# Performance work log

Hardware: AMD Instinct MI355X
Metric: run time of the kernel (lower is better)

## Reference

```python
import jax, jax.numpy as jnp
import numpy as np

B, S, D, H, HD, F, V = 16, 512, 256, 8, 32, 682, 32000
EPS = 1.1920928955078125e-07


def rmsnorm(x, w):
    return x * jax.lax.rsqrt(jnp.mean(x * x, axis=-1, keepdims=True) + EPS) * w


def rope(x, cos, sin):
    # interleaved RoPE: even/odd lanes rotated pairwise, re-interleaved
    xe, xo = x[..., ::2], x[..., 1::2]
    return jnp.stack([xe * cos - xo * sin, xe * sin + xo * cos], axis=-1).reshape(x.shape)


def setup_inputs() -> dict:
    key = jax.random.key(0)
    ks = jax.random.split(key, 12)
    def n(k, shape, s=0.02):
        return jax.random.normal(k, shape, jnp.float32) * s
    pos = jnp.arange(S, dtype=jnp.float32)
    inv = 1.0 / (10000.0 ** (jnp.arange(0, HD, 2, dtype=jnp.float32) / HD))
    ang = pos[:, None] * inv[None, :]                      # [S, HD/2]
    cos_tab = jnp.repeat(jnp.cos(ang), 2, axis=-1)         # [S, HD]
    sin_tab = jnp.repeat(jnp.sin(ang), 2, axis=-1)
    mask = jnp.tril(jnp.ones((S, S), jnp.int32))[None, None]  # causal [1,1,S,S]
    return dict(
        emb=n(ks[0], (V, D)),
        pos_emb=n(ks[1], (S, D)),
        attn_norm_w=jnp.ones((D,), jnp.float32),
        wq=n(ks[2], (D, D)), bq=jnp.zeros((D,), jnp.float32),
        wk=n(ks[3], (HD, D)), bk=jnp.zeros((HD,), jnp.float32),
        wv=n(ks[4], (D, D)), bv=jnp.zeros((D,), jnp.float32),
        cos_tab=cos_tab, sin_tab=sin_tab,
        ffn_norm_w=jnp.ones((D,), jnp.float32),
        w_gate=n(ks[5], (F, D)), b_gate=jnp.zeros((F,), jnp.float32),
        w_up=n(ks[6], (F, D)), b_up=jnp.zeros((F,), jnp.float32),
        w_down=n(ks[7], (D, F)), b_down=jnp.zeros((D,), jnp.float32),
        tok_ids=jax.random.randint(ks[8], (B, S), 0, V, jnp.int64),
        mask=mask,
    )


def reference(emb, pos_emb, attn_norm_w, wq, bq, wk, bk, wv, bv, cos_tab, sin_tab,
              ffn_norm_w, w_gate, b_gate, w_up, b_up, w_down, b_down, tok_ids, mask):
    h = emb[tok_ids] + pos_emb                                   # [B,S,D]
    x = rmsnorm(h, attn_norm_w)
    # faithful to trace: direct view [B,S,D] -> [B,H,S,HD] (no transpose)
    q = (x @ wq.T + bq).reshape(B, H, S, HD)
    k = (x @ wk.T + bk)[:, None]                                 # [B,1,S,HD] single KV head
    v = (x @ wv.T + bv).reshape(B, H, S, HD)
    cos = cos_tab[:S, ::2][None, None]                           # [1,1,S,HD/2]
    sin = sin_tab[:S, ::2][None, None]
    qr = rope(q, cos, sin)
    kr = rope(k, cos, sin)[:, 0]                                 # [B,S,HD]
    scores = jnp.einsum('bhsd,btd->bhst', qr, kr) / jnp.sqrt(jnp.float32(HD))
    scores = jnp.where(mask == 0, -jnp.inf, scores)
    attn = jax.nn.softmax(scores, axis=-1)
    o = jnp.einsum('bhst,bhtd->bhsd', attn, v).reshape(B, S, D)
    h2 = o + h
    x2 = rmsnorm(h2, ffn_norm_w)
    g = x2 @ w_gate.T + b_gate
    g = g * jax.nn.sigmoid(g)                                    # SiLU gate
    up = x2 @ w_up.T + b_up
    out = (g * up) @ w_down.T + b_down
    # faithful to trace: residual uses post-norm activation x2, not h2
    return out + x2
```

## Files before the change

### kernel.cpp

```cpp
#include <hip/hip_runtime.h>
#include <hip/hip_bf16.h>
#include <cstddef>
#include <cstdint>

constexpr int Bb = 16, Ss = 512, Dd = 256, Hh = 8, HDd = 32, Ff = 682;
constexpr int FKp = 704;
constexpr float EPSf = 1.1920928955078125e-07f;

typedef short bf8v __attribute__((ext_vector_type(8)));
typedef float f4 __attribute__((ext_vector_type(4)));
using bf16 = __hip_bfloat16;

__device__ inline f4 MFMA(bf8v a, bf8v b, f4 c) {
  return __builtin_amdgcn_mfma_f32_16x16x32_bf16(a, b, c, 0, 0, 0);
}

__global__ __launch_bounds__(256) void k_embed_norm(
    const float* __restrict__ emb, const float* __restrict__ pos,
    const int* __restrict__ tok, const float* __restrict__ w,
    bf16* __restrict__ hb, bf16* __restrict__ xb)
{
  const int row = blockIdx.x;
  const int s = row & (Ss - 1);
  const int tid = threadIdx.x;
  const int t = tok[row];
  float v = emb[(size_t)t * Dd + tid] + pos[(size_t)s * Dd + tid];
  float ss = v * v;
  #pragma unroll
  for (int off = 32; off > 0; off >>= 1) ss += __shfl_down(ss, off);
  __shared__ float red[4];
  if ((tid & 63) == 0) red[tid >> 6] = ss;
  __syncthreads();
  const float tot = red[0] + red[1] + red[2] + red[3];
  const float r = rsqrtf(tot * (1.0f / Dd) + EPSf);
  const size_t o = (size_t)row * Dd + tid;
  hb[o] = __float2bfloat16(v);
  xb[o] = __float2bfloat16(v * r * w[tid]);
}

__global__ __launch_bounds__(256) void k_add_norm(
    const bf16* __restrict__ a, const bf16* __restrict__ hb,
    const float* __restrict__ w, bf16* __restrict__ x2b)
{
  const int row = blockIdx.x;
  const int tid = threadIdx.x;
  const size_t off = (size_t)row * Dd + tid;
  const float v = __bfloat162float(a[off]) + __bfloat162float(hb[off]);
  float ss = v * v;
  #pragma unroll
  for (int o = 32; o > 0; o >>= 1) ss += __shfl_down(ss, o);
  __shared__ float red[4];
  if ((tid & 63) == 0) red[tid >> 6] = ss;
  __syncthreads();
  const float tot = red[0] + red[1] + red[2] + red[3];
  const float r = rsqrtf(tot * (1.0f / Dd) + EPSf);
  x2b[off] = __float2bfloat16(v * r * w[tid]);
}

__global__ __launch_bounds__(256) void k_cvt_all(
    const float* __restrict__ wq, const float* __restrict__ wk,
    const float* __restrict__ wv, const float* __restrict__ wg,
    const float* __restrict__ wu, const float* __restrict__ wd,
    bf16* __restrict__ dqkv, bf16* __restrict__ dgate,
    bf16* __restrict__ dup, bf16* __restrict__ ddown)
{
  const int b = blockIdx.x, tid = threadIdx.x;
  if (b < 640) {
    const int idx = b * 256 + tid;
    const int row = idx >> 8, col = idx & 255;
    float v;
    if (row < 256)      v = wq[(size_t)row * 256 + col];
    else if (row < 288) v = wk[(size_t)(row - 256) * 256 + col];
    else if (row < 544) v = wv[(size_t)(row - 288) * 256 + col];
    else                v = 0.f;
    dqkv[idx] = __float2bfloat16(v);
  } else if (b < 2176) {
    const bool isg = b < 1408;
    const int idx = (b - (isg ? 640 : 1408)) * 256 + tid;
    const int row = idx >> 8, col = idx & 255;
    const float* src = isg ? wg : wu;
    float v = (row < Ff) ? src[(size_t)row * 256 + col] : 0.f;
    (isg ? dgate : dup)[idx] = __float2bfloat16(v);
  } else {
    const int idx = (b - 2176) * 256 + tid;
    const int row = idx / FKp, col = idx - row * FKp;
    float v = (col < Ff) ? wd[(size_t)row * Ff + col] : 0.f;
    ddown[idx] = __float2bfloat16(v);
  }
}

__global__ __launch_bounds__(256) void k_qkv(
    const bf16* __restrict__ A, const bf16* __restrict__ W,
    const float* __restrict__ bias0, const float* __restrict__ bias1,
    const float* __restrict__ bias2,
    const float* __restrict__ cost, const float* __restrict__ sint,
    bf16* __restrict__ ob0, bf16* __restrict__ ob1, bf16* __restrict__ vt)
{
  __shared__ bf16 As[128 * 72];
  __shared__ bf16 Bs[64 * 72];
  const int tid = threadIdx.x, lane = tid & 63, wid = tid >> 6;
  const int l15 = lane & 15, lg = lane >> 4;
  const int m0 = blockIdx.x * 128, n0 = blockIdx.y * 64;
  const int wr = (wid >> 1) * 64, wc = (wid & 1) * 32;
  const int srow = tid >> 3, scol = (tid & 7) * 8;

  f4 acc[4][2];
  #pragma unroll
  for (int i = 0; i < 4; i++)
    #pragma unroll
    for (int j = 0; j < 2; j++) acc[i][j] = (f4){0.f, 0.f, 0.f, 0.f};

  bf8v pa[4], pb[2];
  #pragma unroll
  for (int i = 0; i < 4; i++)
    pa[i] = *(const bf8v*)&A[(size_t)(m0 + srow + i * 32) * 256 + scol];
  #pragma unroll
  for (int i = 0; i < 2; i++)
    pb[i] = *(const bf8v*)&W[(size_t)(n0 + srow + i * 32) * 256 + scol];
  #pragma unroll
  for (int i = 0; i < 4; i++) *(bf8v*)&As[(srow + i * 32) * 72 + scol] = pa[i];
  #pragma unroll
  for (int i = 0; i < 2; i++) *(bf8v*)&Bs[(srow + i * 32) * 72 + scol] = pb[i];
  __syncthreads();

  for (int ks = 0; ks < 4; ks++) {
    if (ks < 3) {
      const int kn = (ks + 1) * 64;
      #pragma unroll
      for (int i = 0; i < 4; i++)
        pa[i] = *(const bf8v*)&A[(size_t)(m0 + srow + i * 32) * 256 + kn + scol];
      #pragma unroll
      for (int i = 0; i < 2; i++)
        pb[i] = *(const bf8v*)&W[(size_t)(n0 + srow + i * 32) * 256 + kn + scol];
    }
    #pragma unroll
    for (int kk = 0; kk < 64; kk += 32) {
      bf8v af[4], bw[2];
      #pragma unroll
      for (int mi = 0; mi < 4; mi++)
        af[mi] = *(const bf8v*)&As[(wr + mi * 16 + l15) * 72 + kk + lg * 8];
      #pragma unroll
      for (int ni = 0; ni < 2; ni++)
        bw[ni] = *(const bf8v*)&Bs[(wc + ni * 16 + l15) * 72 + kk + lg * 8];
      #pragma unroll
      for (int mi = 0; mi < 4; mi++)
        #pragma unroll
        for (int ni = 0; ni < 2; ni++)
          acc[mi][ni] = MFMA(af[mi], bw[ni], acc[mi][ni]);
    }
    __syncthreads();
    if (ks < 3) {
      #pragma unroll
      for (int i = 0; i < 4; i++) *(bf8v*)&As[(srow + i * 32) * 72 + scol] = pa[i];
      #pragma unroll
      for (int i = 0; i < 2; i++) *(bf8v*)&Bs[(srow + i * 32) * 72 + scol] = pb[i];
      __syncthreads();
    }
  }

  #pragma unroll
  for (int mi = 0; mi < 4; mi++) {
    #pragma unroll
    for (int ni = 0; ni < 2; ni++) {
      const int nbase = n0 + wc + ni * 16;
      const int n = nbase + l15;
      if (nbase < 288) {
        #pragma unroll
        for (int r = 0; r < 4; r++) {
          const int m = m0 + wr + mi * 16 + lg * 4 + r;
          float vb2 = acc[mi][ni][r] + (nbase < 256 ? bias0[n] : bias1[n - 256]);
          int s, hd;
          if (nbase < 256) { const int flat = ((m & 511) << 8) + n; s = (flat >> 5) & 511; hd = n & 31; }
          else             { s = m & 511; hd = n - 256; }
          const float c = cost[s * 32 + hd], sn = sint[s * 32 + hd];
          const float other = __shfl_xor(vb2, 1);
          const float res = (n & 1) ? (other * sn + vb2 * c) : (vb2 * c - other * sn);
          if (nbase < 256) ob0[(size_t)m * 256 + n] = __float2bfloat16(res);
          else             ob1[(size_t)m * 32 + hd] = __float2bfloat16(res);
        }
      } else if (nbase < 544) {
        const int rel = n - 288;
        const int hd = rel & 31, rq = rel >> 5;
        const int mb = m0 + wr + mi * 16 + lg * 4;
        const int b = mb >> 9;
        const float bv = bias2[rel];
        #pragma unroll
        for (int r = 0; r < 4; r++) {
          const int s = (mb + r) & 511;
          const int hh2 = s >> 6;
          const int s4 = ((s & 63) << 3) + rq;
          vt[((size_t)(b * Hh + hh2) * HDd + hd) * Ss + s4] =
              __float2bfloat16(acc[mi][ni][r] + bv);
        }
      }
    }
  }
}

__global__ __launch_bounds__(256) void k_ffn(
    const bf16* __restrict__ A, const bf16* __restrict__ Wg,
    const bf16* __restrict__ Wu,
    const float* __restrict__ bg, const float* __restrict__ bu,
    bf16* __restrict__ out)
{
  __shared__ bf16 As[128 * 72];
  __shared__ bf16 Gs[64 * 72];
  __shared__ bf16 Us[64 * 72];
  const int tid = threadIdx.x, lane = tid & 63, wid = tid >> 6;
  const int l15 = lane & 15, lg = lane >> 4;
  const int m0 = blockIdx.x * 128, n0 = blockIdx.y * 64;
  const int wr = (wid >> 1) * 64, wc = (wid & 1) * 32;
  const int srow = tid >> 3, scol = (tid & 7) * 8;

  f4 accg[4][2], accu[4][2];
  #pragma unroll
  for (int i = 0; i < 4; i++)
    #pragma unroll
    for (int j = 0; j < 2; j++) {
      accg[i][j] = (f4){0.f, 0.f, 0.f, 0.f};
      accu[i][j] = (f4){0.f, 0.f, 0.f, 0.f};
    }

  bf8v pa[4], pg[2], pu[2];
  #pragma unroll
  for (int i = 0; i < 4; i++)
    pa[i] = *(const bf8v*)&A[(size_t)(m0 + srow + i * 32) * 256 + scol];
  #pragma unroll
  for (int i = 0; i < 2; i++) {
    pg[i] = *(const bf8v*)&Wg[(size_t)(n0 + srow + i * 32) * 256 + scol];
    pu[i] = *(const bf8v*)&Wu[(size_t)(n0 + srow + i * 32) * 256 + scol];
  }
  #pragma unroll
  for (int i = 0; i < 4; i++) *(bf8v*)&As[(srow + i * 32) * 72 + scol] = pa[i];
  #pragma unroll
  for (int i = 0; i < 2; i++) {
    *(bf8v*)&Gs[(srow + i * 32) * 72 + scol] = pg[i];
    *(bf8v*)&Us[(srow + i * 32) * 72 + scol] = pu[i];
  }
  __syncthreads();

  for (int ks = 0; ks < 4; ks++) {
    if (ks < 3) {
      const int kn = (ks + 1) * 64;
      #pragma unroll
      for (int i = 0; i < 4; i++)
        pa[i] = *(const bf8v*)&A[(size_t)(m0 + srow + i * 32) * 256 + kn + scol];
      #pragma unroll
      for (int i = 0; i < 2; i++) {
        pg[i] = *(const bf8v*)&Wg[(size_t)(n0 + srow + i * 32) * 256 + kn + scol];
        pu[i] = *(const bf8v*)&Wu[(size_t)(n0 + srow + i * 32) * 256 + kn + scol];
      }
    }
    #pragma unroll
    for (int kk = 0; kk < 64; kk += 32) {
      bf8v af[4], bgf[2], buf[2];
      #pragma unroll
      for (int mi = 0; mi < 4; mi++)
        af[mi] = *(const bf8v*)&As[(wr + mi * 16 + l15) * 72 + kk + lg * 8];
      #pragma unroll
      for (int ni = 0; ni < 2; ni++) {
        bgf[ni] = *(const bf8v*)&Gs[(wc + ni * 16 + l15) * 72 + kk + lg * 8];
        buf[ni] = *(const bf8v*)&Us[(wc + ni * 16 + l15) * 72 + kk + lg * 8];
      }
      #pragma unroll
      for (int mi = 0; mi < 4; mi++)
        #pragma unroll
        for (int ni = 0; ni < 2; ni++) {
          accg[mi][ni] = MFMA(af[mi], bgf[ni], accg[mi][ni]);
          accu[mi][ni] = MFMA(af[mi], buf[ni], accu[mi][ni]);
        }
    }
    __syncthreads();
    if (ks < 3) {
      #pragma unroll
      for (int i = 0; i < 4; i++) *(bf8v*)&As[(srow + i * 32) * 72 + scol] = pa[i];
      #pragma unroll
      for (int i = 0; i < 2; i++) {
        *(bf8v*)&Gs[(srow + i * 32) * 72 + scol] = pg[i];
        *(bf8v*)&Us[(srow + i * 32) * 72 + scol] = pu[i];
      }
      __syncthreads();
    }
  }

  #pragma unroll
  for (int ni = 0; ni < 2; ni++) {
    const int n = n0 + wc + ni * 16 + l15;
    const float bgv = (n < Ff) ? bg[n] : 0.f;
    const float buv = (n < Ff) ? bu[n] : 0.f;
    #pragma unroll
    for (int mi = 0; mi < 4; mi++) {
      #pragma unroll
      for (int r = 0; r < 4; r++) {
        const int m = m0 + wr + mi * 16 + lg * 4 + r;
        float res = 0.f;
        if (n < Ff) {
          const float gv = accg[mi][ni][r] + bgv;
          const float uv = accu[mi][ni][r] + buv;
          res = gv / (1.f + __expf(-gv)) * uv;
        }
        out[(size_t)m * FKp + n] = __float2bfloat16(res);
      }
    }
  }
}

__global__ __launch_bounds__(256) void k_down(
    const bf16* __restrict__ A, const bf16* __restrict__ W,
    const float* __restrict__ bias, const bf16* __restrict__ resid,
    float* __restrict__ out)
{
  __shared__ bf16 As[64 * 72];
  __shared__ bf16 Bs[64 * 72];
  const int tid = threadIdx.x, lane = tid & 63, wid = tid >> 6;
  const int l15 = lane & 15, lg = lane >> 4;
  const int m0 = blockIdx.x * 64, n0 = blockIdx.y * 64;
  const int wr = (wid >> 1) * 32, wc = (wid & 1) * 32;
  const int srow = tid >> 3, scol = (tid & 7) * 8;

  f4 acc[2][2];
  #pragma unroll
  for (int i = 0; i < 2; i++)
    #pragma unroll
    for (int j = 0; j < 2; j++) acc[i][j] = (f4){0.f, 0.f, 0.f, 0.f};

  bf8v pa[2], pb[2];
  #pragma unroll
  for (int i = 0; i < 2; i++) {
    pa[i] = *(const bf8v*)&A[(size_t)(m0 + srow + i * 32) * FKp + scol];
    pb[i] = *(const bf8v*)&W[(size_t)(n0 + srow + i * 32) * FKp + scol];
  }
  #pragma unroll
  for (int i = 0; i < 2; i++) {
    *(bf8v*)&As[(srow + i * 32) * 72 + scol] = pa[i];
    *(bf8v*)&Bs[(srow + i * 32) * 72 + scol] = pb[i];
  }
  __syncthreads();

  for (int ks = 0; ks < 11; ks++) {
    if (ks < 10) {
      const int kn = (ks + 1) * 64;
      #pragma unroll
      for (int i = 0; i < 2; i++) {
        pa[i] = *(const bf8v*)&A[(size_t)(m0 + srow + i * 32) * FKp + kn + scol];
        pb[i] = *(const bf8v*)&W[(size_t)(n0 + srow + i * 32) * FKp + kn + scol];
      }
    }
    #pragma unroll
    for (int kk = 0; kk < 64; kk += 32) {
      bf8v af[2], bw[2];
      #pragma unroll
      for (int mi = 0; mi < 2; mi++)
        af[mi] = *(const bf8v*)&As[(wr + mi * 16 + l15) * 72 + kk + lg * 8];
      #pragma unroll
      for (int ni = 0; ni < 2; ni++)
        bw[ni] = *(const bf8v*)&Bs[(wc + ni * 16 + l15) * 72 + kk + lg * 8];
      #pragma unroll
      for (int mi = 0; mi < 2; mi++)
        #pragma unroll
        for (int ni = 0; ni < 2; ni++)
          acc[mi][ni] = MFMA(af[mi], bw[ni], acc[mi][ni]);
    }
    __syncthreads();
    if (ks < 10) {
      #pragma unroll
      for (int i = 0; i < 2; i++) {
        *(bf8v*)&As[(srow + i * 32) * 72 + scol] = pa[i];
        *(bf8v*)&Bs[(srow + i * 32) * 72 + scol] = pb[i];
      }
      __syncthreads();
    }
  }

  #pragma unroll
  for (int ni = 0; ni < 2; ni++) {
    const int n = n0 + wc + ni * 16 + l15;
    const float bv = bias[n];
    #pragma unroll
    for (int mi = 0; mi < 2; mi++) {
      #pragma unroll
      for (int r = 0; r < 4; r++) {
        const int m = m0 + wr + mi * 16 + lg * 4 + r;
        out[(size_t)m * 256 + n] = acc[mi][ni][r] + bv +
            __bfloat162float(resid[(size_t)m * 256 + n]);
      }
    }
  }
}

__global__ __launch_bounds__(256) void k_attn_mfma(
    const bf16* __restrict__ q, const bf16* __restrict__ k,
    const bf16* __restrict__ vt, bf16* __restrict__ o)
{
  __shared__ bf16 Ps[4][2][16 * 72];
  const int tid = threadIdx.x, lane = tid & 63, wid = tid >> 6;
  const int l15 = lane & 15, lg = lane >> 4;
  const int hh = blockIdx.y, bb = blockIdx.z;
  const int bh = bb * Hh + hh;
  const int gw = blockIdx.x * 4 + wid;
  const int qrw[2] = {gw * 16, 496 - gw * 16};
  const int lt[2] = {(qrw[0] + 15) >> 6, (qrw[1] + 15) >> 6};
  const float scale = 0.17677669529663687f;

  const bf16* kg = k + (size_t)bb * Ss * HDd;
  const bf16* vg = vt + (size_t)bh * (Ss * HDd);

  bf8v qf[2];
  #pragma unroll
  for (int qi = 0; qi < 2; qi++)
    qf[qi] = *(const bf8v*)&q[((size_t)bh * Ss + qrw[qi] + l15) * HDd + lg * 8];

  f4 oacc[2][2];
  float mr[2][4], lr[2][4];
  #pragma unroll
  for (int qi = 0; qi < 2; qi++) {
    oacc[qi][0] = (f4){0.f, 0.f, 0.f, 0.f};
    oacc[qi][1] = (f4){0.f, 0.f, 0.f, 0.f};
    #pragma unroll
    for (int r = 0; r < 4; r++) { mr[qi][r] = -3.0e38f; lr[qi][r] = 0.f; }
  }

  for (int ti = 0; ti <= lt[1]; ti++) {
    const int t0 = ti * 64;
    const bool act0 = (ti <= lt[0]);

    f4 sf[2][4];
    __builtin_amdgcn_s_setprio(1);
    #pragma unroll
    for (int tf = 0; tf < 4; tf++) {
      const bf8v kf = *(const bf8v*)&kg[(size_t)(t0 + tf * 16 + l15) * HDd + lg * 8];
      sf[1][tf] = MFMA(qf[1], kf, (f4){0.f, 0.f, 0.f, 0.f});
      if (act0) sf[0][tf] = MFMA(qf[0], kf, (f4){0.f, 0.f, 0.f, 0.f});
    }
    __builtin_amdgcn_s_setprio(0);

    bf8v vb[2][2];
    #pragma unroll
    for (int kt = 0; kt < 2; kt++)
      #pragma unroll
      for (int hf = 0; hf < 2; hf++)
        vb[kt][hf] = *(const bf8v*)&vg[(size_t)(hf * 16 + l15) * Ss + t0 + kt * 32 + lg * 8];

    #pragma unroll
    for (int qi = 0; qi < 2; qi++) {
      if (qi == 0 && !act0) continue;
      const int qr = qrw[qi];
      const bool diag = (ti == lt[qi]);
      float pm[4] = {-3.0e38f, -3.0e38f, -3.0e38f, -3.0e38f};
      #pragma unroll
      for (int tf = 0; tf < 4; tf++)
        #pragma unroll
        for (int r = 0; r < 4; r++) {
          float sv = sf[qi][tf][r] * scale;
          if (diag && (t0 + tf * 16 + l15 > qr + lg * 4 + r)) sv = -3.0e38f;
          sf[qi][tf][r] = sv;
          pm[r] = fmaxf(pm[r], sv);
        }
      float corr[4];
      #pragma unroll
      for (int r = 0; r < 4; r++) {
        #pragma unroll
        for (int x = 1; x < 16; x <<= 1) pm[r] = fmaxf(pm[r], __shfl_xor(pm[r], x));
        const float nm = fmaxf(mr[qi][r], pm[r]);
        corr[r] = __expf(mr[qi][r] - nm);
        mr[qi][r] = nm;
      }
      float lsum[4] = {0.f, 0.f, 0.f, 0.f};
      #pragma unroll
      for (int tf = 0; tf < 4; tf++)
        #pragma unroll
        for (int r = 0; r < 4; r++) {
          const float p = __expf(sf[qi][tf][r] - mr[qi][r]);
          sf[qi][tf][r] = p;
          lsum[r] += p;
        }
      #pragma unroll
      for (int tf = 0; tf < 4; tf++)
        #pragma unroll
        for (int r = 0; r < 4; r++)
          Ps[wid][qi][(lg * 4 + r) * 72 + tf * 16 + l15] = __float2bfloat16(sf[qi][tf][r]);
      #pragma unroll
      for (int r = 0; r < 4; r++) {
        #pragma unroll
        for (int x = 1; x < 16; x <<= 1) lsum[r] += __shfl_xor(lsum[r], x);
        lr[qi][r] = lr[qi][r] * corr[r] + lsum[r];
      }
      #pragma unroll
      for (int hf = 0; hf < 2; hf++)
        #pragma unroll
        for (int r = 0; r < 4; r++) oacc[qi][hf][r] *= corr[r];

      __builtin_amdgcn_s_setprio(1);
      #pragma unroll
      for (int kt = 0; kt < 2; kt++) {
        const bf8v pv = *(const bf8v*)&Ps[wid][qi][l15 * 72 + kt * 32 + lg * 8];
        #pragma unroll
        for (int hf = 0; hf < 2; hf++)
          oacc[qi][hf] = MFMA(pv, vb[kt][hf], oacc[qi][hf]);
      }
      __builtin_amdgcn_s_setprio(0);
    }
  }

  #pragma unroll
  for (int qi = 0; qi < 2; qi++)
    #pragma unroll
    for (int hf = 0; hf < 2; hf++)
      #pragma unroll
      for (int r = 0; r < 4; r++)
        o[((size_t)bh * Ss + qrw[qi] + lg * 4 + r) * HDd + hf * 16 + l15] =
            __float2bfloat16(oacc[qi][hf][r] / lr[qi][r]);
}

extern "C" void kernel_launch(void* const* d_in, const int* in_sizes, int n_in,
                              void* d_out, int out_size, void* d_ws, size_t ws_size,
                              hipStream_t stream)
{
  const float* emb     = (const float*)d_in[0];
  const float* pos_emb = (const float*)d_in[1];
  const float* attn_w  = (const float*)d_in[2];
  const float* wq      = (const float*)d_in[3];
  const float* bq      = (const float*)d_in[4];
  const float* wk      = (const float*)d_in[5];
  const float* bk      = (const float*)d_in[6];
  const float* wv      = (const float*)d_in[7];
  const float* bv      = (const float*)d_in[8];
  const float* cos_t   = (const float*)d_in[9];
  const float* sin_t   = (const float*)d_in[10];
  const float* ffn_w   = (const float*)d_in[11];
  const float* w_gate  = (const float*)d_in[12];
  const float* b_gate  = (const float*)d_in[13];
  const float* w_up    = (const float*)d_in[14];
  const float* b_up    = (const float*)d_in[15];
  const float* w_down  = (const float*)d_in[16];
  const float* b_down  = (const float*)d_in[17];
  const int*   tok     = (const int*)d_in[18];
  float* out = (float*)d_out;

  const size_t NT = (size_t)Bb * Ss;
  char* base = (char*)d_ws;
  size_t off = 0;
  auto alloc = [&](size_t bytes) {
    void* r = base + off;
    off = (off + bytes + 255) & ~(size_t)255;
    return r;
  };
  bf16*  h_bf   = (bf16*)alloc(NT * Dd * 2);
  bf16*  x_bf   = (bf16*)alloc(NT * Dd * 2);
  bf16*  q_bf   = (bf16*)alloc(NT * Dd * 2);
  bf16*  k_bf   = (bf16*)alloc(NT * HDd * 2);
  bf16*  vt_bf  = (bf16*)alloc(NT * Dd * 2);
  bf16*  o_bf   = (bf16*)alloc(NT * Dd * 2);
  bf16*  x2_bf  = (bf16*)alloc(NT * Dd * 2);
  bf16*  g_bf   = (bf16*)alloc(NT * (size_t)FKp * 2);
  bf16*  wqkv_b = (bf16*)alloc((size_t)640 * 256 * 2);
  bf16*  wgate_b= (bf16*)alloc((size_t)768 * 256 * 2);
  bf16*  wup_b  = (bf16*)alloc((size_t)768 * 256 * 2);
  bf16*  wdown_b= (bf16*)alloc((size_t)256 * FKp * 2);

  k_cvt_all<<<dim3(2880), 256, 0, stream>>>(
      wq, wk, wv, w_gate, w_up, w_down, wqkv_b, wgate_b, wup_b, wdown_b);

  k_embed_norm<<<dim3(NT), 256, 0, stream>>>(emb, pos_emb, tok, attn_w, h_bf, x_bf);

  k_qkv<<<dim3(NT / 128, 10), 256, 0, stream>>>(
      x_bf, wqkv_b, bq, bk, bv, cos_t, sin_t, q_bf, k_bf, vt_bf);

  k_attn_mfma<<<dim3(4, Hh, Bb), 256, 0, stream>>>(q_bf, k_bf, vt_bf, o_bf);

  k_add_norm<<<dim3(NT), 256, 0, stream>>>(o_bf, h_bf, ffn_w, x2_bf);

  k_ffn<<<dim3(NT / 128, 11), 256, 0, stream>>>(
      x2_bf, wgate_b, wup_b, b_gate, b_up, g_bf);

  k_down<<<dim3(NT / 64, 4), 256, 0, stream>>>(
      g_bf, wdown_b, b_down, x2_bf, out);
}
```

Before: 94.76 us.

## Merge weight conversion with embed-norm and restructure attention into one-wave blocks

The weight-conversion and embedding+RMSNorm kernels are merged into one launch, which removes a kernel boundary. Attention now runs one 64-thread wave per block, with each wave handling a single 16-row query tile instead of a balanced pair of tiles. Blocks are issued with the longest causal tiles first. Scores are computed transposed (K as the A operand), so the softmax reduction uses two cross-lane shuffles instead of four, and the P tile is written to LDS in vector chunks. The trade-off is losing the paired load balancing and launching many more small blocks.

```diff
diff --git a/kernel.cpp b/kernel.cpp
--- a/kernel.cpp
+++ b/kernel.cpp
@@ -15,54 +15,15 @@
   return __builtin_amdgcn_mfma_f32_16x16x32_bf16(a, b, c, 0, 0, 0);
 }
 
-__global__ __launch_bounds__(256) void k_embed_norm(
-    const float* __restrict__ emb, const float* __restrict__ pos,
-    const int* __restrict__ tok, const float* __restrict__ w,
-    bf16* __restrict__ hb, bf16* __restrict__ xb)
-{
-  const int row = blockIdx.x;
-  const int s = row & (Ss - 1);
-  const int tid = threadIdx.x;
-  const int t = tok[row];
-  float v = emb[(size_t)t * Dd + tid] + pos[(size_t)s * Dd + tid];
-  float ss = v * v;
-  #pragma unroll
-  for (int off = 32; off > 0; off >>= 1) ss += __shfl_down(ss, off);
-  __shared__ float red[4];
-  if ((tid & 63) == 0) red[tid >> 6] = ss;
-  __syncthreads();
-  const float tot = red[0] + red[1] + red[2] + red[3];
-  const float r = rsqrtf(tot * (1.0f / Dd) + EPSf);
-  const size_t o = (size_t)row * Dd + tid;
-  hb[o] = __float2bfloat16(v);
-  xb[o] = __float2bfloat16(v * r * w[tid]);
-}
-
-__global__ __launch_bounds__(256) void k_add_norm(
-    const bf16* __restrict__ a, const bf16* __restrict__ hb,
-    const float* __restrict__ w, bf16* __restrict__ x2b)
-{
-  const int row = blockIdx.x;
-  const int tid = threadIdx.x;
-  const size_t off = (size_t)row * Dd + tid;
-  const float v = __bfloat162float(a[off]) + __bfloat162float(hb[off]);
-  float ss = v * v;
-  #pragma unroll
-  for (int o = 32; o > 0; o >>= 1) ss += __shfl_down(ss, o);
-  __shared__ float red[4];
-  if ((tid & 63) == 0) red[tid >> 6] = ss;
-  __syncthreads();
-  const float tot = red[0] + red[1] + red[2] + red[3];
-  const float r = rsqrtf(tot * (1.0f / Dd) + EPSf);
-  x2b[off] = __float2bfloat16(v * r * w[tid]);
-}
-
-__global__ __launch_bounds__(256) void k_cvt_all(
+__global__ __launch_bounds__(256) void k_prep(
     const float* __restrict__ wq, const float* __restrict__ wk,
     const float* __restrict__ wv, const float* __restrict__ wg,
     const float* __restrict__ wu, const float* __restrict__ wd,
     bf16* __restrict__ dqkv, bf16* __restrict__ dgate,
-    bf16* __restrict__ dup, bf16* __restrict__ ddown)
+    bf16* __restrict__ dup, bf16* __restrict__ ddown,
+    const float* __restrict__ emb, const float* __restrict__ pos,
+    const int* __restrict__ tok, const float* __restrict__ w,
+    bf16* __restrict__ hb, bf16* __restrict__ xb)
 {
   const int b = blockIdx.x, tid = threadIdx.x;
   if (b < 640) {
@@ -81,12 +42,47 @@
     const float* src = isg ? wg : wu;
     float v = (row < Ff) ? src[(size_t)row * 256 + col] : 0.f;
     (isg ? dgate : dup)[idx] = __float2bfloat16(v);
-  } else {
+  } else if (b < 2880) {
     const int idx = (b - 2176) * 256 + tid;
     const int row = idx / FKp, col = idx - row * FKp;
     float v = (col < Ff) ? wd[(size_t)row * Ff + col] : 0.f;
     ddown[idx] = __float2bfloat16(v);
-  }
+  } else {
+    const int row = b - 2880;
+    const int s = row & (Ss - 1);
+    const int t = tok[row];
+    float v = emb[(size_t)t * Dd + tid] + pos[(size_t)s * Dd + tid];
+    float ss = v * v;
+    #pragma unroll
+    for (int off = 32; off > 0; off >>= 1) ss += __shfl_down(ss, off);
+    __shared__ float red[4];
+    if ((tid & 63) == 0) red[tid >> 6] = ss;
+    __syncthreads();
+    const float tot = red[0] + red[1] + red[2] + red[3];
+    const float r = rsqrtf(tot * (1.0f / Dd) + EPSf);
+    const size_t o = (size_t)row * Dd + tid;
+    hb[o] = __float2bfloat16(v);
+    xb[o] = __float2bfloat16(v * r * w[tid]);
+  }
+}
+
+__global__ __launch_bounds__(256) void k_add_norm(
+    const bf16* __restrict__ a, const bf16* __restrict__ hb,
+    const float* __restrict__ w, bf16* __restrict__ x2b)
+{
+  const int row = blockIdx.x;
+  const int tid = threadIdx.x;
+  const size_t off = (size_t)row * Dd + tid;
+  const float v = __bfloat162float(a[off]) + __bfloat162float(hb[off]);
+  float ss = v * v;
+  #pragma unroll
+  for (int o = 32; o > 0; o >>= 1) ss += __shfl_down(ss, o);
+  __shared__ float red[4];
+  if ((tid & 63) == 0) red[tid >> 6] = ss;
+  __syncthreads();
+  const float tot = red[0] + red[1] + red[2] + red[3];
+  const float r = rsqrtf(tot * (1.0f / Dd) + EPSf);
+  x2b[off] = __float2bfloat16(v * r * w[tid]);
 }
 
 __global__ __launch_bounds__(256) void k_qkv(
@@ -388,49 +384,38 @@
   }
 }
 
-__global__ __launch_bounds__(256) void k_attn_mfma(
+__global__ __launch_bounds__(64) void k_attn_mfma(
     const bf16* __restrict__ q, const bf16* __restrict__ k,
     const bf16* __restrict__ vt, bf16* __restrict__ o)
 {
-  __shared__ bf16 Ps[4][2][16 * 72];
-  const int tid = threadIdx.x, lane = tid & 63, wid = tid >> 6;
+  __shared__ bf16 Ps[16 * 72];
+  const int lane = threadIdx.x;
   const int l15 = lane & 15, lg = lane >> 4;
   const int hh = blockIdx.y, bb = blockIdx.z;
   const int bh = bb * Hh + hh;
-  const int gw = blockIdx.x * 4 + wid;
-  const int qrw[2] = {gw * 16, 496 - gw * 16};
-  const int lt[2] = {(qrw[0] + 15) >> 6, (qrw[1] + 15) >> 6};
+  const int qrow = (31 - blockIdx.x) * 16;
+  const int lt = (qrow + 15) >> 6;
   const float scale = 0.17677669529663687f;
 
   const bf16* kg = k + (size_t)bb * Ss * HDd;
   const bf16* vg = vt + (size_t)bh * (Ss * HDd);
 
-  bf8v qf[2];
-  #pragma unroll
-  for (int qi = 0; qi < 2; qi++)
-    qf[qi] = *(const bf8v*)&q[((size_t)bh * Ss + qrw[qi] + l15) * HDd + lg * 8];
-
-  f4 oacc[2][2];
-  float mr[2][4], lr[2][4];
-  #pragma unroll
-  for (int qi = 0; qi < 2; qi++) {
-    oacc[qi][0] = (f4){0.f, 0.f, 0.f, 0.f};
-    oacc[qi][1] = (f4){0.f, 0.f, 0.f, 0.f};
-    #pragma unroll
-    for (int r = 0; r < 4; r++) { mr[qi][r] = -3.0e38f; lr[qi][r] = 0.f; }
-  }
-
-  for (int ti = 0; ti <= lt[1]; ti++) {
+  const bf8v qf = *(const bf8v*)&q[((size_t)bh * Ss + qrow + l15) * HDd + lg * 8];
+
+  f4 oacc[2];
+  oacc[0] = (f4){0.f, 0.f, 0.f, 0.f};
+  oacc[1] = (f4){0.f, 0.f, 0.f, 0.f};
+  float m = -3.0e38f, l = 0.f;
+
+  for (int ti = 0; ti <= lt; ti++) {
     const int t0 = ti * 64;
-    const bool act0 = (ti <= lt[0]);
-
-    f4 sf[2][4];
+
+    f4 sf[4];
     __builtin_amdgcn_s_setprio(1);
     #pragma unroll
     for (int tf = 0; tf < 4; tf++) {
       const bf8v kf = *(const bf8v*)&kg[(size_t)(t0 + tf * 16 + l15) * HDd + lg * 8];
-      sf[1][tf] = MFMA(qf[1], kf, (f4){0.f, 0.f, 0.f, 0.f});
-      if (act0) sf[0][tf] = MFMA(qf[0], kf, (f4){0.f, 0.f, 0.f, 0.f});
+      sf[tf] = MFMA(kf, qf, (f4){0.f, 0.f, 0.f, 0.f});
     }
     __builtin_amdgcn_s_setprio(0);
 
@@ -441,75 +426,83 @@
       for (int hf = 0; hf < 2; hf++)
         vb[kt][hf] = *(const bf8v*)&vg[(size_t)(hf * 16 + l15) * Ss + t0 + kt * 32 + lg * 8];
 
-    #pragma unroll
-    for (int qi = 0; qi < 2; qi++) {
-      if (qi == 0 && !act0) continue;
-      const int qr = qrw[qi];
-      const bool diag = (ti == lt[qi]);
-      float pm[4] = {-3.0e38f, -3.0e38f, -3.0e38f, -3.0e38f};
+    float pm = -3.0e38f;
+    if (ti == lt) {
       #pragma unroll
       for (int tf = 0; tf < 4; tf++)
         #pragma unroll
         for (int r = 0; r < 4; r++) {
-          float sv = sf[qi][tf][r] * scale;
-          if (diag && (t0 + tf * 16 + l15 > qr + lg * 4 + r)) sv = -3.0e38f;
-          sf[qi][tf][r] = sv;
-          pm[r] = fmaxf(pm[r], sv);
+          float sv = sf[tf][r] * scale;
+          if (t0 + tf * 16 + lg * 4 + r > qrow + l15) sv = -3.0e38f;
+          sf[tf][r] = sv;
+          pm = fmaxf(pm, sv);
         }
-      float corr[4];
+    } else {
+      #pragma unroll
+      for (int tf = 0; tf < 4; tf++)
+        #pragma unroll
+        for (int r = 0; r < 4; r++) {
+          const float sv = sf[tf][r] * scale;
+          sf[tf][r] = sv;
+          pm = fmaxf(pm, sv);
+        }
+    }
+    pm = fmaxf(pm, __shfl_xor(pm, 16));
+    pm = fmaxf(pm, __shfl_xor(pm, 32));
+
+    const float nm = fmaxf(m, pm);
+    const float corr = __expf(m - nm);
+    m = nm;
+
+    float ls = 0.f;
+    #pragma unroll
+    for (int tf = 0; tf < 4; tf++)
       #pragma unroll
       for (int r = 0; r < 4; r++) {
-        #pragma unroll
-        for (int x = 1; x < 16; x <<= 1) pm[r] = fmaxf(pm[r], __shfl_xor(pm[r], x));
-        const float nm = fmaxf(mr[qi][r], pm[r]);
-        corr[r] = __expf(mr[qi][r] - nm);
-        mr[qi][r] = nm;
-      }
-      float lsum[4] = {0.f, 0.f, 0.f, 0.f};
-      #pragma unroll
-      for (int tf = 0; tf < 4; tf++)
-        #pragma unroll
-        for (int r = 0; r < 4; r++) {
-          const float p = __expf(sf[qi][tf][r] - mr[qi][r]);
-          sf[qi][tf][r] = p;
-          lsum[r] += p;
-        }
-      #pragma unroll
-      for (int tf = 0; tf < 4; tf++)
-        #pragma unroll
-        for (int r = 0; r < 4; r++)
-          Ps[wid][qi][(lg * 4 + r) * 72 + tf * 16 + l15] = __float2bfloat16(sf[qi][tf][r]);
-      #pragma unroll
-      for (int r = 0; r < 4; r++) {
-        #pragma unroll
-        for (int x = 1; x < 16; x <<= 1) lsum[r] += __shfl_xor(lsum[r], x);
-        lr[qi][r] = lr[qi][r] * corr[r] + lsum[r];
-      }
+        const float p = __expf(sf[tf][r] - m);
+        sf[tf][r] = p;
+        ls += p;
+      }
+    ls += __shfl_xor(ls, 16);
+    ls += __shfl_xor(ls, 32);
+    l = l * corr + ls;
+
+    #pragma unroll
+    for (int tf = 0; tf < 4; tf++) {
+      bf16 t4[4];
+      #pragma unroll
+      for (int r = 0; r < 4; r++) t4[r] = __float2bfloat16(sf[tf][r]);
+      *(uint2*)&Ps[l15 * 72 + tf * 16 + lg * 4] = *(const uint2*)t4;
+    }
+
+    float corrT[4];
+    #pragma unroll
+    for (int r = 0; r < 4; r++) corrT[r] = __shfl(corr, lg * 4 + r);
+    #pragma unroll
+    for (int hf = 0; hf < 2; hf++)
+      #pragma unroll
+      for (int r = 0; r < 4; r++) oacc[hf][r] *= corrT[r];
+
+    __builtin_amdgcn_s_setprio(1);
+    #pragma unroll
+    for (int kt = 0; kt < 2; kt++) {
+      const bf8v pv = *(const bf8v*)&Ps[l15 * 72 + kt * 32 + lg * 8];
       #pragma unroll
       for (int hf = 0; hf < 2; hf++)
-        #pragma unroll
-        for (int r = 0; r < 4; r++) oacc[qi][hf][r] *= corr[r];
-
-      __builtin_amdgcn_s_setprio(1);
-      #pragma unroll
-      for (int kt = 0; kt < 2; kt++) {
-        const bf8v pv = *(const bf8v*)&Ps[wid][qi][l15 * 72 + kt * 32 + lg * 8];
-        #pragma unroll
-        for (int hf = 0; hf < 2; hf++)
-          oacc[qi][hf] = MFMA(pv, vb[kt][hf], oacc[qi][hf]);
-      }
-      __builtin_amdgcn_s_setprio(0);
-    }
-  }
-
-  #pragma unroll
-  for (int qi = 0; qi < 2; qi++)
-    #pragma unroll
-    for (int hf = 0; hf < 2; hf++)
-      #pragma unroll
-      for (int r = 0; r < 4; r++)
-        o[((size_t)bh * Ss + qrw[qi] + lg * 4 + r) * HDd + hf * 16 + l15] =
-            __float2bfloat16(oacc[qi][hf][r] / lr[qi][r]);
+        oacc[hf] = MFMA(pv, vb[kt][hf], oacc[hf]);
+    }
+    __builtin_amdgcn_s_setprio(0);
+  }
+
+  float lT[4];
+  #pragma unroll
+  for (int r = 0; r < 4; r++) lT[r] = __shfl(l, lg * 4 + r);
+  #pragma unroll
+  for (int hf = 0; hf < 2; hf++)
+    #pragma unroll
+    for (int r = 0; r < 4; r++)
+      o[((size_t)bh * Ss + qrow + lg * 4 + r) * HDd + hf * 16 + l15] =
+          __float2bfloat16(oacc[hf][r] / lT[r]);
 }
 
 extern "C" void kernel_launch(void* const* d_in, const int* in_sizes, int n_in,
@@ -558,15 +551,14 @@
   bf16*  wup_b  = (bf16*)alloc((size_t)768 * 256 * 2);
   bf16*  wdown_b= (bf16*)alloc((size_t)256 * FKp * 2);
 
-  k_cvt_all<<<dim3(2880), 256, 0, stream>>>(
-      wq, wk, wv, w_gate, w_up, w_down, wqkv_b, wgate_b, wup_b, wdown_b);
-
-  k_embed_norm<<<dim3(NT), 256, 0, stream>>>(emb, pos_emb, tok, attn_w, h_bf, x_bf);
+  k_prep<<<dim3(2880 + NT), 256, 0, stream>>>(
+      wq, wk, wv, w_gate, w_up, w_down, wqkv_b, wgate_b, wup_b, wdown_b,
+      emb, pos_emb, tok, attn_w, h_bf, x_bf);
 
   k_qkv<<<dim3(NT / 128, 10), 256, 0, stream>>>(
       x_bf, wqkv_b, bq, bk, bv, cos_t, sin_t, q_bf, k_bf, vt_bf);
 
-  k_attn_mfma<<<dim3(4, Hh, Bb), 256, 0, stream>>>(q_bf, k_bf, vt_bf, o_bf);
+  k_attn_mfma<<<dim3(32, Hh, Bb), 64, 0, stream>>>(q_bf, k_bf, vt_bf, o_bf);
 
   k_add_norm<<<dim3(NT), 256, 0, stream>>>(o_bf, h_bf, ffn_w, x2_bf);
 
```

After: 90.47 us. 1.05x faster.
